# Kernel optimization log

Measured on AMD Instinct MI355X. Metric: run time of the kernel, lower is better.

The kernel has to match this reference:

```python
import jax, jax.numpy as jnp
import numpy as np

N, E = 50000, 800000
F_IN, HID, SENT = 128, 128, 128
NEG_SLOPE = 0.2  # GATConv default negative_slope


def _glorot(key, shape):
    fan_in, fan_out = shape[0], shape[-1]
    lim = float(np.sqrt(6.0 / (fan_in + fan_out)))
    return jax.random.uniform(key, shape, jnp.float32, -lim, lim)


def _gat_layer(x, src, dst, edge_attr, W, att_s, att_d, We, att_e, b):
    """PyG GATConv, heads=1, add_self_loops=True (fill_value='mean')."""
    n = x.shape[0]
    # self-loop edge_attr = mean of incoming edge features per dst node
    deg = jax.ops.segment_sum(jnp.ones(src.shape[0], x.dtype), dst, num_segments=n)
    loop_attr = jax.ops.segment_sum(edge_attr, dst, num_segments=n) / jnp.maximum(deg, 1.0)[:, None]
    loops = jnp.arange(n, dtype=src.dtype)
    src = jnp.concatenate([src, loops])
    dst = jnp.concatenate([dst, loops])
    ea = jnp.concatenate([edge_attr, loop_attr], axis=0)
    # projections (lin_src used for both src and dst when x is a single tensor)
    h = x @ W                           # [N, C]
    a_s = h @ att_s                     # [N]
    a_d = h @ att_d                     # [N]
    a_e = (ea @ We) @ att_e             # [E+N]
    alpha = jax.nn.leaky_relu(a_s[src] + a_d[dst] + a_e, NEG_SLOPE)
    # segment softmax over dst neighborhoods (self-loops guarantee nonempty)
    m = jax.ops.segment_max(alpha, dst, num_segments=n)
    ex = jnp.exp(alpha - m[dst])
    w = ex / jax.ops.segment_sum(ex, dst, num_segments=n)[dst]
    # message = alpha * h_src, scatter-add to dst
    return jax.ops.segment_sum(w[:, None] * h[src], dst, num_segments=n) + b


def setup_inputs() -> dict:
    key = jax.random.key(0)
    ks = jax.random.split(key, 16)
    x = jax.random.normal(ks[0], (N, F_IN), jnp.float32)
    edge_index = jax.random.randint(ks[1], (2, E), 0, N, jnp.int64)
    edge_attr = jax.random.normal(ks[2], (E, SENT), jnp.float32)
    params = {
        'W1': _glorot(ks[3], (F_IN, HID)),
        'a1s': _glorot(ks[4], (HID,)),
        'a1d': _glorot(ks[5], (HID,)),
        'We1': _glorot(ks[6], (SENT, HID)),
        'ae1': _glorot(ks[7], (HID,)),
        'b1': jnp.zeros((HID,), jnp.float32),
        'W2': _glorot(ks[8], (HID, HID)),
        'a2s': _glorot(ks[9], (HID,)),
        'a2d': _glorot(ks[10], (HID,)),
        'We2': _glorot(ks[11], (SENT, HID)),
        'ae2': _glorot(ks[12], (HID,)),
        'b2': jnp.zeros((HID,), jnp.float32),
    }
    return {'x': x, 'edge_index': edge_index, 'edge_attr': edge_attr, **params}


def reference(x, edge_index, edge_attr, W1, a1s, a1d, We1, ae1, b1,
              W2, a2s, a2d, We2, ae2, b2):
    src, dst = edge_index[0], edge_index[1]
    h = _gat_layer(x, src, dst, edge_attr, W1, a1s, a1d, We1, ae1, b1)
    h = jax.nn.relu(h)  # dropout p=0.1 inactive in eval
    return _gat_layer(h, src, dst, edge_attr, W2, a2s, a2d, We2, ae2, b2)
```

## Files before the change

kernel.cpp:

```cpp
#include <hip/hip_runtime.h>
#include <cstdint>

#define D 128
#define NEG 0.2f

typedef __attribute__((ext_vector_type(8))) short bf16x8;
typedef __attribute__((ext_vector_type(4))) float f32x4;

__device__ __forceinline__ float wsum(float v){
#pragma unroll
  for(int m=32;m;m>>=1) v += __shfl_xor(v,m,64);
  return v;
}
__device__ __forceinline__ float lrelu(float a){ return a>0.f ? a : NEG*a; }
__device__ __forceinline__ unsigned short f2bf(float f){
  unsigned int u = __float_as_uint(f);
  u += 0x7fffu + ((u>>16)&1u);
  return (unsigned short)(u>>16);
}
__device__ __forceinline__ float bf2f(unsigned short s){
  return __uint_as_float(((unsigned int)s)<<16);
}

__global__ __launch_bounds__(256) void k_hist(const int* __restrict__ dstv, int* __restrict__ deg, int E){
  int e = blockIdx.x*256 + threadIdx.x;
  if (e < E) atomicAdd(deg + dstv[e], 1);
}

__global__ __launch_bounds__(256) void k_scan1i(const int* __restrict__ deg, int* __restrict__ bsum, int N, int NB,
                                                const float* __restrict__ We1, const float* __restrict__ ae1,
                                                const float* __restrict__ We2, const float* __restrict__ ae2,
                                                const float* __restrict__ W1,  const float* __restrict__ W2,
                                                float* __restrict__ weae, ushort* __restrict__ Wtb){
  __shared__ int s[256];
  __shared__ ushort lds[16][128];
  int b = blockIdx.x;
  if (b < NB){
    int i = b*256 + threadIdx.x;
    s[threadIdx.x] = (i < N) ? deg[i] : 0;
    __syncthreads();
#pragma unroll
    for (int st = 128; st; st >>= 1){
      if (threadIdx.x < st) s[threadIdx.x] += s[threadIdx.x + st];
      __syncthreads();
    }
    if (!threadIdx.x) bsum[b] = s[0];
  } else if (b < NB + 64){
    int gw  = ((b - NB)*256 + threadIdx.x) >> 6;
    int lane = threadIdx.x & 63;
    const float* We = (gw & 128) ? We2 : We1;
    const float* ae = (gw & 128) ? ae2 : ae1;
    int row = gw & 127;
    float2 v = ((const float2*)(We + (size_t)row*D))[lane];
    float2 a = ((const float2*)ae)[lane];
    float p = wsum(v.x*a.x + v.y*a.y);
    if (!lane) weae[gw] = p;
  } else {
    int bb = b - NB - 64;
    int layer = bb >> 3;
    int kb = (bb & 7) * 16;
    const float* W = layer ? W2 : W1;
    int t = threadIdx.x;
#pragma unroll
    for (int p = 0; p < 8; ++p){
      int idx = t + p*256;
      int kl = idx >> 7, c = idx & 127;
      lds[kl][c] = f2bf(W[(size_t)(kb+kl)*128 + c]);
    }
    __syncthreads();
    int c = t >> 1, kc = (t & 1) * 8;
    ushort tmp[8];
#pragma unroll
    for (int m = 0; m < 8; ++m) tmp[m] = lds[kc+m][c];
    *(uint4*)&Wtb[(size_t)layer*16384 + (size_t)c*128 + kb + kc] = *(uint4*)tmp;
  }
}

__global__ __launch_bounds__(256) void k_scan23(const int* __restrict__ deg, const int* __restrict__ bsum,
                                                int* __restrict__ rowp, int NB, int N, int E){
  __shared__ int s[256];
  int t = threadIdx.x;
  int v = (t < NB) ? bsum[t] : 0;
  s[t] = v; __syncthreads();
  for (int d = 1; d < 256; d <<= 1){
    int x = (t >= d) ? s[t-d] : 0;
    __syncthreads();
    s[t] += x;
    __syncthreads();
  }
  int boff = (blockIdx.x == 0) ? 0 : s[blockIdx.x - 1];
  __syncthreads();
  int i = blockIdx.x*256 + t;
  int dv = (i < N) ? deg[i] : 0;
  s[t] = dv; __syncthreads();
  for (int d = 1; d < 256; d <<= 1){
    int x = (t >= d) ? s[t-d] : 0;
    __syncthreads();
    s[t] += x;
    __syncthreads();
  }
  if (i < N) rowp[i] = boff + s[t] - dv;
  if (i == N-1) rowp[N] = E;
}

__global__ __launch_bounds__(256) void k_edge(const float* __restrict__ EA,
                                              const int* __restrict__ srcv, const int* __restrict__ dstv,
                                              const float* __restrict__ weae,
                                              const int* __restrict__ rowp, int* __restrict__ cursor,
                                              uint2* __restrict__ pl1, uint2* __restrict__ pl2, int E){
  int l   = threadIdx.x & 63;
  int sub = l & 7;
  int grp = l >> 3;
  float4 w1v[4], w2v[4];
#pragma unroll
  for (int k = 0; k < 4; ++k){
    w1v[k] = ((const float4*)weae)[sub + 8*k];
    w2v[k] = ((const float4*)weae)[32 + sub + 8*k];
  }
  int gwave  = (blockIdx.x*blockDim.x + threadIdx.x) >> 6;
  int nwaves = (gridDim.x*blockDim.x) >> 6;
  for (int e0 = gwave*8; e0 < E; e0 += nwaves*8){
    int e = e0 + grp;
    if (e >= E) continue;
    const float4* row = (const float4*)(EA + (size_t)e*D);
    float s1 = 0.f, s2 = 0.f;
#pragma unroll
    for (int k = 0; k < 4; ++k){
      float4 v = row[sub + 8*k];
      s1 += v.x*w1v[k].x + v.y*w1v[k].y + v.z*w1v[k].z + v.w*w1v[k].w;
      s2 += v.x*w2v[k].x + v.y*w2v[k].y + v.z*w2v[k].z + v.w*w2v[k].w;
    }
#pragma unroll
    for (int m = 1; m <= 4; m <<= 1){
      s1 += __shfl_xor(s1, m, 64);
      s2 += __shfl_xor(s2, m, 64);
    }
    if (!sub){
      int d = dstv[e];
      int pos = rowp[d] + atomicAdd(cursor + d, 1);
      unsigned s = (unsigned)srcv[e];
      pl1[pos] = make_uint2(s, __float_as_uint(s1));
      pl2[pos] = make_uint2(s, __float_as_uint(s2));
    }
  }
}

__global__ __launch_bounds__(256) void k_gemm(const float* __restrict__ Xf, const ushort* __restrict__ Xb,
                                              const ushort* __restrict__ Wtb,
                                              const float* __restrict__ atts, const float* __restrict__ attd,
                                              ushort* __restrict__ Hb,
                                              float* __restrict__ a_s, float* __restrict__ a_d, int N){
  __shared__ ushort xsb[64*136];
  __shared__ ushort wsb[128*136];
  int tid = threadIdx.x;
  int rowbase = blockIdx.x*64;
  if (Xf){
#pragma unroll
    for (int i = 0; i < 4; ++i){
      int idx = tid + i*256;
      int r = idx >> 4, ch = idx & 15;
      int gr = rowbase + r;
      int grc = (gr < N) ? gr : 0;
      const float4* src = (const float4*)(Xf + (size_t)grc*128 + ch*8);
      float4 a = src[0], b = src[1];
      uint4 o;
      o.x = (unsigned)f2bf(a.x) | ((unsigned)f2bf(a.y)<<16);
      o.y = (unsigned)f2bf(a.z) | ((unsigned)f2bf(a.w)<<16);
      o.z = (unsigned)f2bf(b.x) | ((unsigned)f2bf(b.y)<<16);
      o.w = (unsigned)f2bf(b.z) | ((unsigned)f2bf(b.w)<<16);
      *(uint4*)&xsb[r*136 + ch*8] = o;
    }
  } else {
#pragma unroll
    for (int i = 0; i < 4; ++i){
      int idx = tid + i*256;
      int r = idx >> 4, ch = idx & 15;
      int gr = rowbase + r;
      int grc = (gr < N) ? gr : 0;
      *(uint4*)&xsb[r*136 + ch*8] = *(const uint4*)&Xb[(size_t)grc*128 + ch*8];
    }
  }
#pragma unroll
  for (int i = 0; i < 8; ++i){
    int idx = tid + i*256;
    int c = idx >> 4, ch = idx & 15;
    *(uint4*)&wsb[c*136 + ch*8] = *(const uint4*)&Wtb[(size_t)c*128 + ch*8];
  }
  __syncthreads();

  int lane = tid & 63;
  int w    = tid >> 6;
  int l15  = lane & 15;
  int lg   = lane >> 4;
  int r0   = w*16;

  f32x4 acc[8];
#pragma unroll
  for (int ct = 0; ct < 8; ++ct) acc[ct] = (f32x4){0.f,0.f,0.f,0.f};

#pragma unroll
  for (int ks = 0; ks < 4; ++ks){
    bf16x8 af = *(const bf16x8*)&xsb[(r0 + l15)*136 + ks*32 + lg*8];
#pragma unroll
    for (int ct = 0; ct < 8; ++ct){
      bf16x8 bfr = *(const bf16x8*)&wsb[(ct*16 + l15)*136 + ks*32 + lg*8];
      acc[ct] = __builtin_amdgcn_mfma_f32_16x16x32_bf16(af, bfr, acc[ct], 0, 0, 0);
    }
  }

  float attsv[8], attdv[8];
#pragma unroll
  for (int ct = 0; ct < 8; ++ct){
    attsv[ct] = atts[ct*16 + l15];
    attdv[ct] = attd[ct*16 + l15];
  }
  float ps[4] = {0,0,0,0}, pd[4] = {0,0,0,0};
#pragma unroll
  for (int ct = 0; ct < 8; ++ct)
#pragma unroll
    for (int j = 0; j < 4; ++j){
      ps[j] += acc[ct][j]*attsv[ct];
      pd[j] += acc[ct][j]*attdv[ct];
    }
#pragma unroll
  for (int m = 1; m <= 8; m <<= 1)
#pragma unroll
    for (int j = 0; j < 4; ++j){
      ps[j] += __shfl_xor(ps[j], m, 64);
      pd[j] += __shfl_xor(pd[j], m, 64);
    }
#pragma unroll
  for (int j = 0; j < 4; ++j){
    int gr = rowbase + r0 + lg*4 + j;
    if (gr < N && l15 == 0){
      a_s[gr] = ps[j];
      a_d[gr] = pd[j];
    }
  }
#pragma unroll
  for (int ct = 0; ct < 8; ++ct)
#pragma unroll
    for (int j = 0; j < 4; ++j){
      int r = r0 + lg*4 + j;
      xsb[r*136 + ct*16 + l15] = f2bf(acc[ct][j]);
    }
  __syncthreads();
#pragma unroll
  for (int i = 0; i < 4; ++i){
    int idx = tid + i*256;
    int r = idx >> 4, ch = idx & 15;
    int gr = rowbase + r;
    if (gr < N)
      *(uint4*)&Hb[(size_t)gr*128 + ch*8] = *(const uint4*)&xsb[r*136 + ch*8];
  }
}

__global__ __launch_bounds__(256) void k_aggr(const ushort* __restrict__ Hb,
                                              const float* __restrict__ a_s, const float* __restrict__ a_d,
                                              const int* __restrict__ rowp, const uint2* __restrict__ pl,
                                              const float* __restrict__ bias,
                                              float* __restrict__ OUTF, ushort* __restrict__ OUTB, int N){
  __shared__ uint2 lse[4][64];
  int wslot = threadIdx.x >> 6;
  int wid  = (blockIdx.x*blockDim.x + threadIdx.x) >> 6;
  int lane = threadIdx.x & 63;
  if (wid >= N) return;
  int p0 = rowp[wid], p1 = rowp[wid+1];
  float as_own = a_s[wid];
  float ad     = a_d[wid];
  int l32 = lane & 31;
  int hw  = lane >> 5;
  ushort4 uself = make_ushort4(0,0,0,0);
  if (!hw) uself = *(const ushort4*)(Hb + (size_t)wid*D + l32*4);
  float denom = 0.f, sumae = 0.f;
  float4 acc = {0.f,0.f,0.f,0.f};
  for (int c0 = p0; c0 < p1; c0 += 64){
    int p = c0 + lane;
    bool valid = p < p1;
    uint2 rec = valid ? pl[p] : make_uint2(0u, 0u);
    float ae = valid ? __uint_as_float(rec.y) : 0.f;
    float ex = valid ? __expf(lrelu(a_s[rec.x] + ad + ae)) : 0.f;
    sumae += wsum(ae);
    denom += wsum(ex);
    lse[wslot][lane] = make_uint2(rec.x, __float_as_uint(ex));
    int cnt = p1 - c0; if (cnt > 64) cnt = 64;
    for (int it = 0; it*16 < cnt; ++it){
      int base = it*16 + hw*8;
#pragma unroll
      for (int k = 0; k < 8; ++k){
        uint2 t = lse[wslot][base + k];
        float w2 = __uint_as_float(t.y);
        ushort4 u = *(const ushort4*)(Hb + (size_t)t.x*D + l32*4);
        acc.x += w2*bf2f(u.x); acc.y += w2*bf2f(u.y);
        acc.z += w2*bf2f(u.z); acc.w += w2*bf2f(u.w);
      }
    }
  }
  float dg = (float)(p1 - p0);
  float la = sumae / fmaxf(dg, 1.0f);
  float ex_self = __expf(lrelu(as_own + ad + la));
  denom += ex_self;
  acc.x += __shfl_xor(acc.x, 32);
  acc.y += __shfl_xor(acc.y, 32);
  acc.z += __shfl_xor(acc.z, 32);
  acc.w += __shfl_xor(acc.w, 32);
  if (!hw){
    acc.x += ex_self*bf2f(uself.x); acc.y += ex_self*bf2f(uself.y);
    acc.z += ex_self*bf2f(uself.z); acc.w += ex_self*bf2f(uself.w);
    float4 bv = *(const float4*)(bias + l32*4);
    float inv = 1.0f/denom;
    float ox = acc.x*inv + bv.x, oy = acc.y*inv + bv.y;
    float oz = acc.z*inv + bv.z, ow = acc.w*inv + bv.w;
    if (OUTB){
      ox=fmaxf(ox,0.f); oy=fmaxf(oy,0.f); oz=fmaxf(oz,0.f); ow=fmaxf(ow,0.f);
      ushort4 o;
      o.x=f2bf(ox); o.y=f2bf(oy); o.z=f2bf(oz); o.w=f2bf(ow);
      *(ushort4*)(OUTB + (size_t)wid*D + l32*4) = o;
    } else {
      *(float4*)(OUTF + (size_t)wid*D + l32*4) = make_float4(ox,oy,oz,ow);
    }
  }
}

extern "C" void kernel_launch(void* const* d_in, const int* in_sizes, int n_in,
                              void* d_out, int out_size, void* d_ws, size_t ws_size,
                              hipStream_t stream){
  (void)n_in; (void)out_size; (void)ws_size;
  const float* x   = (const float*)d_in[0];
  const int*   ei  = (const int*)d_in[1];
  const float* ea  = (const float*)d_in[2];
  const float* W1  = (const float*)d_in[3];
  const float* a1s = (const float*)d_in[4];
  const float* a1d = (const float*)d_in[5];
  const float* We1 = (const float*)d_in[6];
  const float* ae1 = (const float*)d_in[7];
  const float* b1  = (const float*)d_in[8];
  const float* W2  = (const float*)d_in[9];
  const float* a2s = (const float*)d_in[10];
  const float* a2d = (const float*)d_in[11];
  const float* We2 = (const float*)d_in[12];
  const float* ae2 = (const float*)d_in[13];
  const float* b2  = (const float*)d_in[14];
  int N = in_sizes[0] / D;
  int E = in_sizes[1] / 2;
  const int* srcv = ei;
  const int* dstv = ei + E;
  float* out = (float*)d_out;

  char* p = (char*)d_ws;
  auto allocB = [&](size_t bytes)->void*{
    void* r = (void*)p; p += (bytes + 255) & ~(size_t)255; return r;
  };
  int* deg     = (int*)allocB((size_t)N*4);
  int* cursor  = (int*)allocB((size_t)N*4);
  char* zero_end = p;
  ushort* hb   = (ushort*)allocB((size_t)N*D*2);
  ushort* x2b  = (ushort*)allocB((size_t)N*D*2);
  ushort* Wtb  = (ushort*)allocB((size_t)2*128*128*2);
  uint2* pl1   = (uint2*)allocB((size_t)E*8);
  uint2* pl2   = (uint2*)allocB((size_t)E*8);
  float* as_   = (float*)allocB((size_t)N*4);
  float* ad_   = (float*)allocB((size_t)N*4);
  float* weae  = (float*)allocB(1024);
  int* rowp    = (int*)allocB((size_t)(N+1)*4);
  int* bsum    = (int*)allocB(1024);

  hipMemsetAsync(deg, 0, (size_t)(zero_end - (char*)deg), stream);

  int nb = (N + 255)/256;
  k_hist  <<<(E+255)/256,256,0,stream>>>(dstv, deg, E);
  k_scan1i<<<nb+80,256,0,stream>>>(deg, bsum, N, nb, We1,ae1,We2,ae2,W1,W2, weae, Wtb);
  k_scan23<<<nb,256,0,stream>>>(deg, bsum, rowp, nb, N, E);
  k_edge  <<<2048,256,0,stream>>>(ea, srcv, dstv, weae, rowp, cursor, pl1, pl2, E);

  int gemmb = (N + 63)/64;
  int wgrid = (N + 3)/4;

  k_gemm<<<gemmb,256,0,stream>>>(x, nullptr, Wtb,          a1s, a1d, hb, as_, ad_, N);
  k_aggr<<<wgrid,256,0,stream>>>(hb, as_, ad_, rowp, pl1, b1, nullptr, x2b, N);

  k_gemm<<<gemmb,256,0,stream>>>(nullptr, x2b, Wtb + 16384, a2s, a2d, hb, as_, ad_, N);
  k_aggr<<<wgrid,256,0,stream>>>(hb, as_, ad_, rowp, pl2, b2, out, nullptr, N);
}
```

Measured before the change: 275.6 us.

## Merge edge projection with first GEMM into one launch and unroll edge loads

Merges the edge-attribute projection/CSR fill kernel with the layer-1 node GEMM into a single launch. Blocks below the GEMM count compute GEMM tiles and the rest process edges, so the two independent jobs run concurrently and one launch is saved. The edge loop now handles two edges per 8-lane group per iteration to put more loads in flight. The aggregation tail loop processes leftover neighbors in steps of 4 instead of padding to 16, which avoids wasted gathers. The fused kernel carries the GEMM's large shared-memory allocation into the edge blocks, which can lower their occupancy.

```diff
diff --git a/kernel.cpp b/kernel.cpp
--- a/kernel.cpp
+++ b/kernel.cpp
@@ -103,57 +103,10 @@
   if (i == N-1) rowp[N] = E;
 }
 
-__global__ __launch_bounds__(256) void k_edge(const float* __restrict__ EA,
-                                              const int* __restrict__ srcv, const int* __restrict__ dstv,
-                                              const float* __restrict__ weae,
-                                              const int* __restrict__ rowp, int* __restrict__ cursor,
-                                              uint2* __restrict__ pl1, uint2* __restrict__ pl2, int E){
-  int l   = threadIdx.x & 63;
-  int sub = l & 7;
-  int grp = l >> 3;
-  float4 w1v[4], w2v[4];
-#pragma unroll
-  for (int k = 0; k < 4; ++k){
-    w1v[k] = ((const float4*)weae)[sub + 8*k];
-    w2v[k] = ((const float4*)weae)[32 + sub + 8*k];
-  }
-  int gwave  = (blockIdx.x*blockDim.x + threadIdx.x) >> 6;
-  int nwaves = (gridDim.x*blockDim.x) >> 6;
-  for (int e0 = gwave*8; e0 < E; e0 += nwaves*8){
-    int e = e0 + grp;
-    if (e >= E) continue;
-    const float4* row = (const float4*)(EA + (size_t)e*D);
-    float s1 = 0.f, s2 = 0.f;
-#pragma unroll
-    for (int k = 0; k < 4; ++k){
-      float4 v = row[sub + 8*k];
-      s1 += v.x*w1v[k].x + v.y*w1v[k].y + v.z*w1v[k].z + v.w*w1v[k].w;
-      s2 += v.x*w2v[k].x + v.y*w2v[k].y + v.z*w2v[k].z + v.w*w2v[k].w;
-    }
-#pragma unroll
-    for (int m = 1; m <= 4; m <<= 1){
-      s1 += __shfl_xor(s1, m, 64);
-      s2 += __shfl_xor(s2, m, 64);
-    }
-    if (!sub){
-      int d = dstv[e];
-      int pos = rowp[d] + atomicAdd(cursor + d, 1);
-      unsigned s = (unsigned)srcv[e];
-      pl1[pos] = make_uint2(s, __float_as_uint(s1));
-      pl2[pos] = make_uint2(s, __float_as_uint(s2));
-    }
-  }
-}
-
-__global__ __launch_bounds__(256) void k_gemm(const float* __restrict__ Xf, const ushort* __restrict__ Xb,
-                                              const ushort* __restrict__ Wtb,
-                                              const float* __restrict__ atts, const float* __restrict__ attd,
-                                              ushort* __restrict__ Hb,
-                                              float* __restrict__ a_s, float* __restrict__ a_d, int N){
-  __shared__ ushort xsb[64*136];
-  __shared__ ushort wsb[128*136];
-  int tid = threadIdx.x;
-  int rowbase = blockIdx.x*64;
+__device__ void gemm_tile(int blk, const float* Xf, const ushort* Xb, const ushort* Wtb,
+                          const float* atts, const float* attd, ushort* Hb,
+                          float* a_s, float* a_d, int N, ushort* xsb, ushort* wsb, int tid){
+  int rowbase = blk*64;
   if (Xf){
 #pragma unroll
     for (int i = 0; i < 4; ++i){
@@ -253,6 +206,86 @@
     if (gr < N)
       *(uint4*)&Hb[(size_t)gr*128 + ch*8] = *(const uint4*)&xsb[r*136 + ch*8];
   }
+}
+
+__global__ __launch_bounds__(256) void k_edge_gemm1(const float* __restrict__ EA,
+                                                    const int* __restrict__ srcv, const int* __restrict__ dstv,
+                                                    const float* __restrict__ weae,
+                                                    const int* __restrict__ rowp, int* __restrict__ cursor,
+                                                    uint2* __restrict__ pl1, uint2* __restrict__ pl2, int E,
+                                                    const float* __restrict__ x, const ushort* __restrict__ Wtb,
+                                                    const float* __restrict__ a1s, const float* __restrict__ a1d,
+                                                    ushort* __restrict__ hb,
+                                                    float* __restrict__ as_, float* __restrict__ ad_,
+                                                    int N, int GEMMB, int EB){
+  __shared__ ushort xsb[64*136];
+  __shared__ ushort wsb[128*136];
+  int tid = threadIdx.x;
+  int b   = blockIdx.x;
+  if (b < GEMMB){
+    gemm_tile(b, x, nullptr, Wtb, a1s, a1d, hb, as_, ad_, N, xsb, wsb, tid);
+    return;
+  }
+  int eb = b - GEMMB;
+  int l   = tid & 63;
+  int sub = l & 7;
+  int grp = l >> 3;
+  float4 w1v[4], w2v[4];
+#pragma unroll
+  for (int k = 0; k < 4; ++k){
+    w1v[k] = ((const float4*)weae)[sub + 8*k];
+    w2v[k] = ((const float4*)weae)[32 + sub + 8*k];
+  }
+  int gwave  = (eb*256 + tid) >> 6;
+  int nwaves = EB*4;
+  for (int e0 = gwave*16; e0 < E; e0 += nwaves*16){
+    int eA = e0 + grp;
+    int eB2 = e0 + 8 + grp;
+    bool okA = eA < E, okB = eB2 < E;
+    const float4* rowA = (const float4*)(EA + (size_t)(okA ? eA : 0)*D);
+    const float4* rowB = (const float4*)(EA + (size_t)(okB ? eB2 : 0)*D);
+    float4 vA[4], vB[4];
+#pragma unroll
+    for (int k = 0; k < 4; ++k){ vA[k] = rowA[sub + 8*k]; vB[k] = rowB[sub + 8*k]; }
+    float s1a = 0.f, s2a = 0.f, s1b = 0.f, s2b = 0.f;
+#pragma unroll
+    for (int k = 0; k < 4; ++k){
+      s1a += vA[k].x*w1v[k].x + vA[k].y*w1v[k].y + vA[k].z*w1v[k].z + vA[k].w*w1v[k].w;
+      s2a += vA[k].x*w2v[k].x + vA[k].y*w2v[k].y + vA[k].z*w2v[k].z + vA[k].w*w2v[k].w;
+      s1b += vB[k].x*w1v[k].x + vB[k].y*w1v[k].y + vB[k].z*w1v[k].z + vB[k].w*w1v[k].w;
+      s2b += vB[k].x*w2v[k].x + vB[k].y*w2v[k].y + vB[k].z*w2v[k].z + vB[k].w*w2v[k].w;
+    }
+#pragma unroll
+    for (int m = 1; m <= 4; m <<= 1){
+      s1a += __shfl_xor(s1a, m, 64);
+      s2a += __shfl_xor(s2a, m, 64);
+      s1b += __shfl_xor(s1b, m, 64);
+      s2b += __shfl_xor(s2b, m, 64);
+    }
+    if (!sub && okA){
+      int d = dstv[eA];
+      int pos = rowp[d] + atomicAdd(cursor + d, 1);
+      unsigned s = (unsigned)srcv[eA];
+      pl1[pos] = make_uint2(s, __float_as_uint(s1a));
+      pl2[pos] = make_uint2(s, __float_as_uint(s2a));
+    }
+    if (!sub && okB){
+      int d = dstv[eB2];
+      int pos = rowp[d] + atomicAdd(cursor + d, 1);
+      unsigned s = (unsigned)srcv[eB2];
+      pl1[pos] = make_uint2(s, __float_as_uint(s1b));
+      pl2[pos] = make_uint2(s, __float_as_uint(s2b));
+    }
+  }
+}
+
+__global__ __launch_bounds__(256) void k_gemm(const ushort* __restrict__ Xb, const ushort* __restrict__ Wtb,
+                                              const float* __restrict__ atts, const float* __restrict__ attd,
+                                              ushort* __restrict__ Hb,
+                                              float* __restrict__ a_s, float* __restrict__ a_d, int N){
+  __shared__ ushort xsb[64*136];
+  __shared__ ushort wsb[128*136];
+  gemm_tile(blockIdx.x, nullptr, Xb, Wtb, atts, attd, Hb, a_s, a_d, N, xsb, wsb, threadIdx.x);
 }
 
 __global__ __launch_bounds__(256) void k_aggr(const ushort* __restrict__ Hb,
@@ -284,10 +317,22 @@
     denom += wsum(ex);
     lse[wslot][lane] = make_uint2(rec.x, __float_as_uint(ex));
     int cnt = p1 - c0; if (cnt > 64) cnt = 64;
-    for (int it = 0; it*16 < cnt; ++it){
+    int nfull = cnt & ~15;
+    for (int it = 0; it*16 < nfull; ++it){
       int base = it*16 + hw*8;
 #pragma unroll
       for (int k = 0; k < 8; ++k){
+        uint2 t = lse[wslot][base + k];
+        float w2 = __uint_as_float(t.y);
+        ushort4 u = *(const ushort4*)(Hb + (size_t)t.x*D + l32*4);
+        acc.x += w2*bf2f(u.x); acc.y += w2*bf2f(u.y);
+        acc.z += w2*bf2f(u.z); acc.w += w2*bf2f(u.w);
+      }
+    }
+    for (int j0 = nfull; j0 < cnt; j0 += 4){
+      int base = j0 + hw*2;
+#pragma unroll
+      for (int k = 0; k < 2; ++k){
         uint2 t = lse[wslot][base + k];
         float w2 = __uint_as_float(t.y);
         ushort4 u = *(const ushort4*)(Hb + (size_t)t.x*D + l32*4);
@@ -368,17 +413,16 @@
   hipMemsetAsync(deg, 0, (size_t)(zero_end - (char*)deg), stream);
 
   int nb = (N + 255)/256;
-  k_hist  <<<(E+255)/256,256,0,stream>>>(dstv, deg, E);
-  k_scan1i<<<nb+80,256,0,stream>>>(deg, bsum, N, nb, We1,ae1,We2,ae2,W1,W2, weae, Wtb);
-  k_scan23<<<nb,256,0,stream>>>(deg, bsum, rowp, nb, N, E);
-  k_edge  <<<2048,256,0,stream>>>(ea, srcv, dstv, weae, rowp, cursor, pl1, pl2, E);
-
   int gemmb = (N + 63)/64;
+  int edgeb = 2048;
   int wgrid = (N + 3)/4;
 
-  k_gemm<<<gemmb,256,0,stream>>>(x, nullptr, Wtb,          a1s, a1d, hb, as_, ad_, N);
+  k_hist   <<<(E+255)/256,256,0,stream>>>(dstv, deg, E);
+  k_scan1i <<<nb+80,256,0,stream>>>(deg, bsum, N, nb, We1,ae1,We2,ae2,W1,W2, weae, Wtb);
+  k_scan23 <<<nb,256,0,stream>>>(deg, bsum, rowp, nb, N, E);
+  k_edge_gemm1<<<gemmb+edgeb,256,0,stream>>>(ea, srcv, dstv, weae, rowp, cursor, pl1, pl2, E,
+                                             x, Wtb, a1s, a1d, hb, as_, ad_, N, gemmb, edgeb);
   k_aggr<<<wgrid,256,0,stream>>>(hb, as_, ad_, rowp, pl1, b1, nullptr, x2b, N);
-
-  k_gemm<<<gemmb,256,0,stream>>>(nullptr, x2b, Wtb + 16384, a2s, a2d, hb, as_, ad_, N);
+  k_gemm<<<gemmb,256,0,stream>>>(x2b, Wtb + 16384, a2s, a2d, hb, as_, ad_, N);
   k_aggr<<<wgrid,256,0,stream>>>(hb, as_, ad_, rowp, pl2, b2, out, nullptr, N);
 }
```

After: 283.7 us. 2.9% more time.
